# Kernel tuning notes

Measured on AMD Instinct MI355X. Metric: run time of the kernel, lower is better.

Reference implementation:

```python
import jax, jax.numpy as jnp
from jax import lax
import numpy as np

B, C, HH, WW = 8, 64, 128, 128
N = HH * WW
EPS = 1e-5


def _roll_h(xn, sign):
    # per-channel cyclic roll along H: out[b,c,h,w] = xn[b,c,(h - sign*c) % H, w]
    _, Cx, Hx, _ = xn.shape
    c = jnp.arange(Cx)[:, None]
    idx = (jnp.arange(Hx)[None, :] - sign * jnp.arange(Cx)[:, None]) % Hx  # (C,H)
    return xn[:, c, idx, :]


def _roll_w(xn, sign):
    return _roll_h(xn.transpose(0, 1, 3, 2), sign).transpose(0, 1, 3, 2)


def _ch_linear(xn, w, b):
    # nn.Linear over the channel dim of a BCHW tensor (token-MLP on (B,N,C))
    return jnp.einsum('bchw,cd->bdhw', xn, w) + b[None, :, None, None]


def _bn(xn, g, b):
    # BatchNorm2d, training-mode stats (biased var over B,H,W)
    m = xn.mean(axis=(0, 2, 3), keepdims=True)
    v = xn.var(axis=(0, 2, 3), keepdims=True)
    return (xn - m) * lax.rsqrt(v + EPS) * g[None, :, None, None] + b[None, :, None, None]


def _dwconv(xn, w, dil, pad):
    return lax.conv_general_dilated(xn, w, (1, 1), ((pad, pad), (pad, pad)),
                                    rhs_dilation=(dil, dil),
                                    dimension_numbers=('NCHW', 'OIHW', 'NCHW'),
                                    feature_group_count=xn.shape[1])


def _pc(xn, w):
    # 1x1 pointwise conv, no bias; w: (C_out, C_in)
    return jnp.einsum('bchw,oc->bohw', xn, w)


def lgff_forward(x, fc1_w, fc1_b, fc2_w, fc2_b, fc3_w, fc3_b, fc4_w, fc4_b,
                 fc5_w, fc5_b, ln_g, ln_b, pc_w, dw_w, dw_b, dw_bn_g, dw_bn_b,
                 dd_w, dd_bn_g, dd_bn_b, se_w1, se_b1, se_w2, se_b2, H, W):
    Bx, Nx, Cx = x.shape
    xn = x.transpose(0, 2, 1).reshape(Bx, Cx, H, W)
    # branch 1: roll+c along H -> fc1 -> GELU -> roll+c along W -> fc2
    a = jax.nn.gelu(_ch_linear(_roll_h(xn, 1), fc1_w, fc1_b), approximate=False)
    x_1 = _ch_linear(_roll_w(a, 1), fc2_w, fc2_b) + xn
    # branch 2: roll-c along W -> fc3 -> GELU -> roll+c along H -> fc4
    b = jax.nn.gelu(_ch_linear(_roll_w(xn, -1), fc3_w, fc3_b), approximate=False)
    x_2 = _ch_linear(_roll_h(b, 1), fc4_w, fc4_b) + xn
    # concat along feature dim (token layout dim=2 == channel dim here), LayerNorm(2C), fc5
    xc = jnp.concatenate([x_1, x_2], axis=1)  # (B, 2C, H, W)
    m = xc.mean(axis=1, keepdims=True)
    v = xc.var(axis=1, keepdims=True)
    xc = (xc - m) * lax.rsqrt(v + EPS) * ln_g[None, :, None, None] + ln_b[None, :, None, None]
    x1 = _ch_linear(xc, fc5_w, fc5_b) + xn
    # conv fusion part
    x2 = _pc(x1, pc_w)
    y = jax.nn.relu(_bn(_dwconv(x2, dw_w, 1, 1) + dw_b[None, :, None, None], dw_bn_g, dw_bn_b))
    y = jax.nn.relu(_bn(_dwconv(y, dd_w, 2, 2), dd_bn_g, dd_bn_b))
    y = _pc(y, pc_w)
    # four branches x3..x6 share identical weights/input -> identical outputs
    x7 = 4.0 * (x2 * y)
    # SE block
    s = x7.mean(axis=(2, 3), keepdims=True)  # (B,C,1,1)
    e = jax.nn.relu(jnp.einsum('bcij,oc->boij', s, se_w1) + se_b1[None, :, None, None])
    e = jax.nn.sigmoid(jnp.einsum('bcij,oc->boij', e, se_w2) + se_b2[None, :, None, None])
    return x7 + x7 * e  # (B, C, H, W)


def setup_inputs():
    key = jax.random.key(0)
    ks = jax.random.split(key, 12)
    r = C // 8
    inp = {
        'x': jax.random.normal(ks[0], (B, N, C), jnp.float32),
        'fc1_w': jax.random.normal(ks[1], (C, C), jnp.float32) * 0.02,
        'fc1_b': jnp.zeros((C,), jnp.float32),
        'fc2_w': jax.random.normal(ks[2], (C, C), jnp.float32) * 0.02,
        'fc2_b': jnp.zeros((C,), jnp.float32),
        'fc3_w': jax.random.normal(ks[3], (C, C), jnp.float32) * 0.02,
        'fc3_b': jnp.zeros((C,), jnp.float32),
        'fc4_w': jax.random.normal(ks[4], (C, C), jnp.float32) * 0.02,
        'fc4_b': jnp.zeros((C,), jnp.float32),
        'fc5_w': jax.random.normal(ks[5], (2 * C, C), jnp.float32) * 0.02,
        'fc5_b': jnp.zeros((C,), jnp.float32),
        'ln_g': jnp.ones((2 * C,), jnp.float32),
        'ln_b': jnp.zeros((2 * C,), jnp.float32),
        'pc_w': jax.random.normal(ks[6], (C, C), jnp.float32) * np.sqrt(2.0 / C).astype(np.float32),
        'dw_w': jax.random.normal(ks[7], (C, 1, 3, 3), jnp.float32) * np.sqrt(2.0 / 9.0).astype(np.float32),
        'dw_b': jnp.zeros((C,), jnp.float32),
        'dw_bn_g': jnp.ones((C,), jnp.float32),
        'dw_bn_b': jnp.zeros((C,), jnp.float32),
        'dd_w': jax.random.normal(ks[8], (C, 1, 3, 3), jnp.float32) * np.sqrt(2.0 / 9.0).astype(np.float32),
        'dd_bn_g': jnp.ones((C,), jnp.float32),
        'dd_bn_b': jnp.zeros((C,), jnp.float32),
        'se_w1': jax.random.normal(ks[9], (r, C), jnp.float32) * np.sqrt(2.0 / r).astype(np.float32),
        'se_b1': jnp.zeros((r,), jnp.float32),
        'se_w2': jax.random.normal(ks[10], (C, r), jnp.float32) * np.sqrt(2.0 / C).astype(np.float32),
        'se_b2': jnp.zeros((C,), jnp.float32),
        'H': HH,
        'W': WW,
    }
    return inp


def reference(x, fc1_w, fc1_b, fc2_w, fc2_b, fc3_w, fc3_b, fc4_w, fc4_b,
              fc5_w, fc5_b, ln_g, ln_b, pc_w, dw_w, dw_b, dw_bn_g, dw_bn_b,
              dd_w, dd_bn_g, dd_bn_b, se_w1, se_b1, se_w2, se_b2, H, W):
    return lgff_forward(x, fc1_w, fc1_b, fc2_w, fc2_b, fc3_w, fc3_b, fc4_w, fc4_b,
                        fc5_w, fc5_b, ln_g, ln_b, pc_w, dw_w, dw_b, dw_bn_g, dw_bn_b,
                        dd_w, dd_bn_g, dd_bn_b, se_w1, se_b1, se_w2, se_b2, H, W)
```

## Files before the change

kernel.cpp:

```cpp
#include <hip/hip_runtime.h>

constexpr int NB  = 8;
constexpr int NC  = 64;
constexpr int NH  = 128;
constexpr int NW  = 128;
constexpr int NHW = NH * NW;
constexpr int CHW = NC * NHW;
constexpr int SZ  = NB * CHW;
constexpr int NPOS = NB * NHW;
constexpr float EPS = 1e-5f;

typedef unsigned short u16;
using bf8   = __attribute__((ext_vector_type(8))) short;
using u16x8 = __attribute__((ext_vector_type(8))) u16;
using u16x4 = __attribute__((ext_vector_type(4))) u16;
using f32x4 = __attribute__((ext_vector_type(4))) float;

static __device__ inline short f2bf(float f) {
    union { float f; unsigned int u; } v; v.f = f;
    unsigned int r = v.u + 0x7fffu + ((v.u >> 16) & 1u);
    return (short)(r >> 16);
}
static __device__ inline float bf2f(u16 u) {
    union { unsigned int i; float f; } v; v.i = ((unsigned int)u) << 16;
    return v.f;
}

__global__ void k_transpose(const float* __restrict__ x, u16* __restrict__ xn,
                            const float* __restrict__ w5, const float* __restrict__ lng,
                            const float* __restrict__ lnb, float* __restrict__ PQ) {
    if (blockIdx.x == 2048) {
        int d = threadIdx.x;
        if (d < 64) {
            float P = 0.f, Q = 0.f;
            for (int c = 0; c < 128; ++c) {
                float wv = w5[c * 64 + d];
                P += lng[c] * wv;
                Q += lnb[c] * wv;
            }
            PQ[d] = P; PQ[64 + d] = Q;
        }
        return;
    }
    __shared__ float t[64 * 65];
    int b   = blockIdx.x >> 8;
    int hw0 = (blockIdx.x & 255) << 6;
    int tid = threadIdx.x;
    #pragma unroll
    for (int k = 0; k < 16; ++k) {
        int idx = tid + (k << 8);
        int c = idx & 63, hwl = idx >> 6;
        t[c * 65 + hwl] = x[((size_t)b * NHW + hw0 + hwl) * NC + c];
    }
    __syncthreads();
    #pragma unroll
    for (int k = 0; k < 16; ++k) {
        int idx = tid + (k << 8);
        int hwl = idx & 63, c = idx >> 6;
        xn[(size_t)(b * NC + c) * NHW + hw0 + hwl] = (u16)f2bf(t[c * 65 + hwl]);
    }
}

__global__ __launch_bounds__(512) void
k_mfc2(const u16* __restrict__ xn,
       const float* __restrict__ w1, const float* __restrict__ b1,
       const float* __restrict__ w3, const float* __restrict__ b3,
       u16* __restrict__ t1, u16* __restrict__ t2) {
    __shared__ short wA[64 * 64];
    __shared__ short wB[64 * 64];
    int tid = threadIdx.x;
    int l = tid & 63, wv = tid >> 6;
    int q = l >> 4, col = l & 15;
    int bid = ((blockIdx.x & 7) << 7) | (blockIdx.x >> 3);

    {
        const float* wsrc = (wv < 4) ? w1 : w3;
        short* wdst = (wv < 4) ? wA : wB;
        int wv4 = wv & 3;
        #pragma unroll
        for (int i = 0; i < 8; ++i) {
            int c0 = wv4 * 2 + i * 8;
            unsigned int pk = (unsigned int)(u16)f2bf(wsrc[c0 * 64 + l]) |
                              ((unsigned int)(u16)f2bf(wsrc[(c0 + 1) * 64 + l]) << 16);
            *(unsigned int*)&wdst[l * 64 + (c0 ^ ((l & 7) << 3))] = pk;
        }
    }
    __syncthreads();

    int p  = bid * 128 + wv * 16 + col;
    int b  = p >> 14;
    int hw = p & (NHW - 1);
    int h  = hw >> 7, w = hw & 127;
    const u16* inb = xn + (size_t)b * CHW;

    f32x4 acc1[4], acc2[4];
    #pragma unroll
    for (int dt = 0; dt < 4; ++dt) {
        acc1[dt] = (f32x4){0.f, 0.f, 0.f, 0.f};
        acc2[dt] = (f32x4){0.f, 0.f, 0.f, 0.f};
    }
    #pragma unroll
    for (int ks = 0; ks < 2; ++ks) {
        bf8 f1, f2;
        #pragma unroll
        for (int j = 0; j < 8; ++j) {
            int c = ks * 32 + q * 8 + j;
            f1[j] = (short)inb[c * NHW + (((h - c) & 127) << 7) + w];
            f2[j] = (short)inb[c * NHW + (h << 7) + ((w + c) & 127)];
        }
        #pragma unroll
        for (int dt = 0; dt < 4; ++dt) {
            int d = dt * 16 + col;
            int wo = (ks * 32 + q * 8) ^ ((d & 7) << 3);
            acc1[dt] = __builtin_amdgcn_mfma_f32_16x16x32_bf16(f1, *(bf8*)&wA[d * 64 + wo], acc1[dt], 0, 0, 0);
            acc2[dt] = __builtin_amdgcn_mfma_f32_16x16x32_bf16(f2, *(bf8*)&wB[d * 64 + wo], acc2[dt], 0, 0, 0);
        }
    }

    int hwst = (bid * 128 + wv * 16 + q * 4) & (NHW - 1);
    size_t ob = (size_t)b * CHW + hwst;
    #pragma unroll
    for (int dt = 0; dt < 4; ++dt) {
        int d = dt * 16 + col;
        float bb1 = b1[d], bb3 = b3[d];
        u16x4 o1v, o2v;
        #pragma unroll
        for (int r = 0; r < 4; ++r) {
            float v1 = acc1[dt][r] + bb1;
            v1 = 0.5f * v1 * (1.f + erff(v1 * 0.70710678118654752f));
            float v2 = acc2[dt][r] + bb3;
            v2 = 0.5f * v2 * (1.f + erff(v2 * 0.70710678118654752f));
            o1v[r] = (u16)f2bf(v1);
            o2v[r] = (u16)f2bf(v2);
        }
        *(u16x4*)&t1[ob + (size_t)d * NHW] = o1v;
        *(u16x4*)&t2[ob + (size_t)d * NHW] = o2v;
    }
}

__global__ __launch_bounds__(512) void
k_ffuse(const u16* __restrict__ t1, const u16* __restrict__ t2,
        const u16* __restrict__ xnb,
        const float* __restrict__ fc2w, const float* __restrict__ fc2b,
        const float* __restrict__ fc4w, const float* __restrict__ fc4b,
        const float* __restrict__ w5, const float* __restrict__ lng,
        const float* __restrict__ PQ, const float* __restrict__ b5,
        u16* __restrict__ x1out) {
    __shared__ short wA[64 * 64];
    __shared__ short wB[64 * 64];
    __shared__ short wG[64 * 128];
    __shared__ short xt[128 * 140];

    int tid = threadIdx.x;
    int l = tid & 63, wv = tid >> 6;
    int q = l >> 4, col = l & 15;
    int bid = ((blockIdx.x & 7) << 7) | (blockIdx.x >> 3);

    {
        const float* wsrc = (wv < 4) ? fc2w : fc4w;
        short* wdst = (wv < 4) ? wA : wB;
        int wv4 = wv & 3;
        #pragma unroll
        for (int i = 0; i < 8; ++i) {
            int c0 = wv4 * 2 + i * 8;
            unsigned int pk = (unsigned int)(u16)f2bf(wsrc[c0 * 64 + l]) |
                              ((unsigned int)(u16)f2bf(wsrc[(c0 + 1) * 64 + l]) << 16);
            *(unsigned int*)&wdst[l * 64 + (c0 ^ ((l & 7) << 3))] = pk;
        }
    }
    #pragma unroll
    for (int i = 0; i < 8; ++i) {
        int c0 = wv * 2 + i * 16;
        unsigned int pk = (unsigned int)(u16)f2bf(lng[c0] * w5[c0 * 64 + l]) |
                          ((unsigned int)(u16)f2bf(lng[c0 + 1] * w5[(c0 + 1) * 64 + l]) << 16);
        *(unsigned int*)&wG[l * 128 + (c0 ^ ((l & 7) << 3))] = pk;
    }
    __syncthreads();

    int p  = bid * 128 + wv * 16 + col;
    int b  = p >> 14;
    int hw = p & (NHW - 1);
    int h  = hw >> 7, w = hw & 127;
    size_t base = (size_t)b * CHW;

    f32x4 acc1[4], acc2[4];
    #pragma unroll
    for (int dt = 0; dt < 4; ++dt) {
        acc1[dt] = (f32x4){0.f, 0.f, 0.f, 0.f};
        acc2[dt] = (f32x4){0.f, 0.f, 0.f, 0.f};
    }
    #pragma unroll
    for (int ks = 0; ks < 2; ++ks) {
        bf8 f1, f2;
        #pragma unroll
        for (int j = 0; j < 8; ++j) {
            int c = ks * 32 + q * 8 + j;
            f1[j] = (short)t1[base + c * NHW + (h << 7) + ((w - c) & 127)];
            f2[j] = (short)t2[base + c * NHW + (((h - c) & 127) << 7) + w];
        }
        #pragma unroll
        for (int dt = 0; dt < 4; ++dt) {
            int d = dt * 16 + col;
            int wo = (ks * 32 + q * 8) ^ ((d & 7) << 3);
            acc1[dt] = __builtin_amdgcn_mfma_f32_16x16x32_bf16(f1, *(bf8*)&wA[d * 64 + wo], acc1[dt], 0, 0, 0);
            acc2[dt] = __builtin_amdgcn_mfma_f32_16x16x32_bf16(f2, *(bf8*)&wB[d * 64 + wo], acc2[dt], 0, 0, 0);
        }
    }

    int hwst = (bid * 128 + wv * 16 + q * 4) & (NHW - 1);
    size_t ob = base + hwst;
    u16x4 xr4[4];
    #pragma unroll
    for (int dt = 0; dt < 4; ++dt)
        xr4[dt] = *(const u16x4*)&xnb[ob + (size_t)(dt * 16 + col) * NHW];

    float s[4] = {0.f, 0.f, 0.f, 0.f}, sq[4] = {0.f, 0.f, 0.f, 0.f};
    int posr = wv * 16 + q * 4;
    #pragma unroll
    for (int dt = 0; dt < 4; ++dt) {
        int d = dt * 16 + col;
        float bb2 = fc2b[d], bb4 = fc4b[d];
        #pragma unroll
        for (int r = 0; r < 4; ++r) {
            float xv = bf2f(xr4[dt][r]);
            float v1 = acc1[dt][r] + bb2 + xv;
            float v2 = acc2[dt][r] + bb4 + xv;
            s[r]  += v1 + v2;
            sq[r] += v1 * v1 + v2 * v2;
            xt[(posr + r) * 140 + d]      = f2bf(v1);
            xt[(posr + r) * 140 + 64 + d] = f2bf(v2);
        }
    }
    #pragma unroll
    for (int off = 1; off < 16; off <<= 1) {
        #pragma unroll
        for (int r = 0; r < 4; ++r) {
            s[r]  += __shfl_xor(s[r], off);
            sq[r] += __shfl_xor(sq[r], off);
        }
    }
    float rstd[4], mr[4];
    #pragma unroll
    for (int r = 0; r < 4; ++r) {
        float m   = s[r] * (1.f / 128.f);
        float var = sq[r] * (1.f / 128.f) - m * m;
        rstd[r] = rsqrtf(var + EPS);
        mr[r]   = m * rstd[r];
    }
    __syncthreads();

    f32x4 acc[4];
    #pragma unroll
    for (int dt = 0; dt < 4; ++dt) acc[dt] = (f32x4){0.f, 0.f, 0.f, 0.f};
    #pragma unroll
    for (int ks = 0; ks < 4; ++ks) {
        bf8 bfr = *(bf8*)&xt[(wv * 16 + col) * 140 + ks * 32 + q * 8];
        #pragma unroll
        for (int dt = 0; dt < 4; ++dt) {
            int d = dt * 16 + col;
            bf8 wfr = *(bf8*)&wG[d * 128 + ((ks * 32 + q * 8) ^ ((d & 7) << 3))];
            acc[dt] = __builtin_amdgcn_mfma_f32_16x16x32_bf16(bfr, wfr, acc[dt], 0, 0, 0);
        }
    }

    #pragma unroll
    for (int dt = 0; dt < 4; ++dt) {
        int d = dt * 16 + col;
        float pqd = PQ[d], pqq = PQ[64 + d], b5d = b5[d];
        u16x4 ov;
        #pragma unroll
        for (int r = 0; r < 4; ++r) {
            float val = rstd[r] * acc[dt][r] + pqq - mr[r] * pqd + b5d + bf2f(xr4[dt][r]);
            ov[r] = (u16)f2bf(val);
        }
        *(u16x4*)&x1out[ob + (size_t)d * NHW] = ov;
    }
}

template<bool BNRELU_IN, bool SEPART>
__global__ __launch_bounds__(512) void
k_mfc(const u16* __restrict__ in, const float* __restrict__ wgt,
      const float* __restrict__ psum, const float* __restrict__ psq,
      const float* __restrict__ bng, const float* __restrict__ bnb,
      const u16* __restrict__ x2in, float* __restrict__ gpart,
      u16* __restrict__ out) {
    __shared__ short wt[64 * 64];
    __shared__ float scl[64], sft[64];
    __shared__ float spart[8][64];
    int tid = threadIdx.x;
    int l = tid & 63, wv = tid >> 6;
    int q = l >> 4, col = l & 15;
    int bid = ((blockIdx.x & 7) << 7) | (blockIdx.x >> 3);

    #pragma unroll
    for (int i = 0; i < 8; ++i) {
        int d = wv * 8 + i;
        wt[d * 64 + (l ^ ((d & 7) << 3))] = f2bf(wgt[d * 64 + l]);
    }
    if (BNRELU_IN && tid < 64) {
        float s = 0.f, qv = 0.f;
        #pragma unroll
        for (int i = 0; i < 32; ++i) {
            int bb = i >> 2, j = i & 3;
            int idx = ((bb * 64 + tid) << 2) + j;
            s += psum[idx]; qv += psq[idx];
        }
        const float inv = 1.f / (float)(NB * NHW);
        float m = s * inv;
        float var = qv * inv - m * m;
        float rs = rsqrtf(var + EPS);
        float sc = rs * bng[tid];
        scl[tid] = sc;
        sft[tid] = bnb[tid] - m * sc;
    }
    __syncthreads();

    int p  = bid * 128 + wv * 16 + col;
    int b  = p >> 14;
    int hw = p & (NHW - 1);
    const u16* inb = in + (size_t)b * CHW;

    f32x4 acc[4];
    #pragma unroll
    for (int dt = 0; dt < 4; ++dt) acc[dt] = (f32x4){0.f, 0.f, 0.f, 0.f};

    #pragma unroll
    for (int ks = 0; ks < 2; ++ks) {
        bf8 bfr;
        #pragma unroll
        for (int j = 0; j < 8; ++j) {
            int c = ks * 32 + q * 8 + j;
            u16 raw = inb[c * NHW + hw];
            if (BNRELU_IN) {
                float v = fmaxf(bf2f(raw) * scl[c] + sft[c], 0.f);
                bfr[j] = f2bf(v);
            } else {
                bfr[j] = (short)raw;
            }
        }
        #pragma unroll
        for (int dt = 0; dt < 4; ++dt) {
            int d = dt * 16 + col;
            bf8 afr = *(bf8*)&wt[d * 64 + ((ks * 32 + q * 8) ^ ((d & 7) << 3))];
            acc[dt] = __builtin_amdgcn_mfma_f32_16x16x32_bf16(bfr, afr, acc[dt], 0, 0, 0);
        }
    }

    int hwst = (bid * 128 + wv * 16 + q * 4) & (NHW - 1);
    size_t ob = (size_t)b * CHW + hwst;
    float pp[4] = {0.f, 0.f, 0.f, 0.f};
    #pragma unroll
    for (int dt = 0; dt < 4; ++dt) {
        int d = dt * 16 + col;
        u16x4 ov;
        #pragma unroll
        for (int r = 0; r < 4; ++r) ov[r] = (u16)f2bf(acc[dt][r]);
        *(u16x4*)&out[ob + (size_t)d * NHW] = ov;
        if (SEPART) {
            u16x4 xv = *(const u16x4*)&x2in[ob + (size_t)d * NHW];
            #pragma unroll
            for (int r = 0; r < 4; ++r) pp[dt] += bf2f(xv[r]) * bf2f(ov[r]);
        }
    }

    if (SEPART) {
        #pragma unroll
        for (int dt = 0; dt < 4; ++dt) {
            pp[dt] += __shfl_xor(pp[dt], 16);
            pp[dt] += __shfl_xor(pp[dt], 32);
        }
        if (l < 16) {
            #pragma unroll
            for (int dt = 0; dt < 4; ++dt) spart[wv][dt * 16 + l] = pp[dt];
        }
        __syncthreads();
        if (tid < 64) {
            float s = 0.f;
            #pragma unroll
            for (int w8 = 0; w8 < 8; ++w8) s += spart[w8][tid];
            gpart[(size_t)bid * 64 + tid] = s;
        }
    }
}

__global__ void k_se_fin(const float* __restrict__ gpart, float* __restrict__ svec) {
    int b = blockIdx.x, c = threadIdx.x;
    float s = 0.f;
    for (int k = 0; k < 128; ++k) s += gpart[(size_t)(b * 128 + k) * 64 + c];
    svec[b * 64 + c] = s * (4.f / (float)NHW);
}

template<int DIL, bool HASBIAS, bool BNIN>
__global__ __launch_bounds__(256) void
k_dwlds(const u16* __restrict__ in, const float* __restrict__ wgt,
        const float* __restrict__ bias,
        const float* __restrict__ psumIn, const float* __restrict__ psqIn,
        const float* __restrict__ bng, const float* __restrict__ bnb,
        u16* __restrict__ out, float* __restrict__ psumOut, float* __restrict__ psqOut) {
    constexpr int STR = 136;
    __shared__ float tile[36 * STR];
    __shared__ float ss[256], sq[256];

    int blk = ((blockIdx.x & 7) << 8) | (blockIdx.x >> 3);
    int q   = blk & 3;
    int bc  = blk >> 2;
    int c   = bc & 63;
    int r0  = q * 32;
    int tid = threadIdx.x;
    const u16* ip = in + (size_t)bc * NHW;

    float scale = 0.f, shift = 0.f;
    if (BNIN) {
        float s = 0.f, qv = 0.f;
        #pragma unroll
        for (int i = 0; i < 32; ++i) {
            int bb = i >> 2, j = i & 3;
            int idx = ((bb * 64 + c) << 2) + j;
            s += psumIn[idx]; qv += psqIn[idx];
        }
        const float inv = 1.f / (float)(NB * NHW);
        float m = s * inv;
        float var = qv * inv - m * m;
        float rs = rsqrtf(var + EPS);
        scale = rs * bng[c];
        shift = bnb[c] - m * scale;
    }

    #pragma unroll 1
    for (int idx = tid; idx < 36 * 16; idx += 256) {
        int lr = idx >> 4, u = idx & 15;
        int gr = r0 - 2 + lr;
        float v[8] = {0.f, 0.f, 0.f, 0.f, 0.f, 0.f, 0.f, 0.f};
        if (gr >= 0 && gr < NH) {
            u16x8 raw = *(const u16x8*)(ip + gr * NW + u * 8);
            #pragma unroll
            for (int j = 0; j < 8; ++j) {
                float f = bf2f(raw[j]);
                if (BNIN) f = fmaxf(f * scale + shift, 0.f);
                v[j] = f;
            }
        }
        *(float4*)&tile[lr * STR + 4 + u * 8]     = make_float4(v[0], v[1], v[2], v[3]);
        *(float4*)&tile[lr * STR + 4 + u * 8 + 4] = make_float4(v[4], v[5], v[6], v[7]);
        if (u == 0)  *(float4*)&tile[lr * STR]       = make_float4(0.f, 0.f, 0.f, 0.f);
        if (u == 15) *(float4*)&tile[lr * STR + 132] = make_float4(0.f, 0.f, 0.f, 0.f);
    }
    __syncthreads();

    float wc[9];
    #pragma unroll
    for (int k = 0; k < 9; ++k) wc[k] = wgt[c * 9 + k];

    int row  = tid >> 3;
    int col0 = (tid & 7) * 16;
    float o[16];
    float bb = HASBIAS ? bias[c] : 0.f;
    #pragma unroll
    for (int j = 0; j < 16; ++j) o[j] = bb;

    #pragma unroll
    for (int i = 0; i < 3; ++i) {
        const float* rp = &tile[(row + 2 + (i - 1) * DIL) * STR + 4 + col0];
        float4 A  = *(const float4*)(rp - 4);
        float4 B0 = *(const float4*)(rp);
        float4 B1 = *(const float4*)(rp + 4);
        float4 B2 = *(const float4*)(rp + 8);
        float4 B3 = *(const float4*)(rp + 12);
        float4 Cc = *(const float4*)(rp + 16);
        float ww[24] = {A.x,A.y,A.z,A.w, B0.x,B0.y,B0.z,B0.w, B1.x,B1.y,B1.z,B1.w,
                        B2.x,B2.y,B2.z,B2.w, B3.x,B3.y,B3.z,B3.w, Cc.x,Cc.y,Cc.z,Cc.w};
        float w0 = wc[3 * i], w1 = wc[3 * i + 1], w2 = wc[3 * i + 2];
        #pragma unroll
        for (int j = 0; j < 16; ++j)
            o[j] += w0 * ww[4 + j - DIL] + w1 * ww[4 + j] + w2 * ww[4 + j + DIL];
    }

    u16* op = out + (size_t)bc * NHW + (r0 + row) * NW + col0;
    u16x8 o1, o2;
    #pragma unroll
    for (int j = 0; j < 8; ++j) { o1[j] = (u16)f2bf(o[j]); o2[j] = (u16)f2bf(o[8 + j]); }
    *(u16x8*)(op)     = o1;
    *(u16x8*)(op + 8) = o2;

    float s = 0.f, qq = 0.f;
    #pragma unroll
    for (int j = 0; j < 16; ++j) { s += o[j]; qq += o[j] * o[j]; }
    ss[tid] = s; sq[tid] = qq; __syncthreads();
    for (int off = 128; off > 0; off >>= 1) {
        if (tid < off) { ss[tid] += ss[tid + off]; sq[tid] += sq[tid + off]; }
        __syncthreads();
    }
    if (tid == 0) { psumOut[blk] = ss[0]; psqOut[blk] = sq[0]; }
}

__global__ void k_final8(const u16* __restrict__ x2, const u16* __restrict__ y3,
                         const float* __restrict__ svec,
                         const float* __restrict__ w1, const float* __restrict__ b1,
                         const float* __restrict__ w2, const float* __restrict__ b2,
                         float* __restrict__ out) {
    __shared__ float sh[64], e1[8], ev[1];
    int tid = threadIdx.x;
    int bc = blockIdx.x >> 3;
    int b  = bc >> 6, c = bc & 63;

    if (tid < 64) sh[tid] = svec[b * 64 + tid];
    __syncthreads();
    if (tid < 8) {
        float a = b1[tid];
        for (int cc = 0; cc < 64; ++cc) a += sh[cc] * w1[tid * 64 + cc];
        e1[tid] = a > 0.f ? a : 0.f;
    }
    __syncthreads();
    if (tid == 0) {
        float a = b2[c];
        #pragma unroll
        for (int j = 0; j < 8; ++j) a += e1[j] * w2[c * 8 + j];
        ev[0] = 1.f / (1.f + expf(-a));
    }
    __syncthreads();

    int t = blockIdx.x * 256 + tid;
    float f = 4.f * (1.f + ev[0]);
    u16x8 av = *(const u16x8*)(x2 + (size_t)t * 8);
    u16x8 bv = *(const u16x8*)(y3 + (size_t)t * 8);
    float4 o0, o1;
    o0.x = f * bf2f(av[0]) * bf2f(bv[0]); o0.y = f * bf2f(av[1]) * bf2f(bv[1]);
    o0.z = f * bf2f(av[2]) * bf2f(bv[2]); o0.w = f * bf2f(av[3]) * bf2f(bv[3]);
    o1.x = f * bf2f(av[4]) * bf2f(bv[4]); o1.y = f * bf2f(av[5]) * bf2f(bv[5]);
    o1.z = f * bf2f(av[6]) * bf2f(bv[6]); o1.w = f * bf2f(av[7]) * bf2f(bv[7]);
    *(float4*)(out + (size_t)t * 8)     = o0;
    *(float4*)(out + (size_t)t * 8 + 4) = o1;
}

extern "C" void kernel_launch(void* const* d_in, const int* in_sizes, int n_in,
                              void* d_out, int out_size, void* d_ws, size_t ws_size,
                              hipStream_t stream) {
    const float* x     = (const float*)d_in[0];
    const float* fc1w  = (const float*)d_in[1];
    const float* fc1b  = (const float*)d_in[2];
    const float* fc2w  = (const float*)d_in[3];
    const float* fc2b  = (const float*)d_in[4];
    const float* fc3w  = (const float*)d_in[5];
    const float* fc3b  = (const float*)d_in[6];
    const float* fc4w  = (const float*)d_in[7];
    const float* fc4b  = (const float*)d_in[8];
    const float* fc5w  = (const float*)d_in[9];
    const float* fc5b  = (const float*)d_in[10];
    const float* lng   = (const float*)d_in[11];
    const float* lnb   = (const float*)d_in[12];
    const float* pcw   = (const float*)d_in[13];
    const float* dww   = (const float*)d_in[14];
    const float* dwb   = (const float*)d_in[15];
    const float* dwbng = (const float*)d_in[16];
    const float* dwbnb = (const float*)d_in[17];
    const float* ddw   = (const float*)d_in[18];
    const float* ddbng = (const float*)d_in[19];
    const float* ddbnb = (const float*)d_in[20];
    const float* sew1  = (const float*)d_in[21];
    const float* seb1  = (const float*)d_in[22];
    const float* sew2  = (const float*)d_in[23];
    const float* seb2  = (const float*)d_in[24];

    float* out = (float*)d_out;
    u16* wsu = (u16*)d_ws;
    u16* bufA = wsu;
    u16* bufB = wsu + (size_t)SZ;
    u16* bufC = wsu + (size_t)2 * SZ;
    u16* bufD = wsu + (size_t)3 * SZ;
    float* st = (float*)(wsu + (size_t)4 * SZ);
    float* psumA = st;
    float* psqA  = st + 2048;
    float* psumB = st + 4096;
    float* psqB  = st + 6144;
    float* svec  = st + 8192;
    float* pqv   = st + 8704;
    float* gpart = st + 8832;

    dim3 blk(256);
    dim3 blk512(512);
    const float* nil = nullptr;
    const u16*   nilu = nullptr;
    float*       nilf = nullptr;

    k_transpose<<<2049, blk, 0, stream>>>(x, bufA, fc5w, lng, lnb, pqv);
    k_mfc2<<<NPOS / 128, blk512, 0, stream>>>(bufA, fc1w, fc1b, fc3w, fc3b, bufB, bufC);
    k_ffuse<<<NPOS / 128, blk512, 0, stream>>>(bufB, bufC, bufA, fc2w, fc2b, fc4w, fc4b,
                                               fc5w, lng, pqv, fc5b, bufD);
    k_mfc<false, false><<<NPOS / 128, blk512, 0, stream>>>(bufD, pcw, nil, nil, nil, nil, nilu, nilf, bufA);
    k_dwlds<1, true, false><<<2048, blk, 0, stream>>>(bufA, dww, dwb, nil, nil, nil, nil, bufB, psumA, psqA);
    k_dwlds<2, false, true><<<2048, blk, 0, stream>>>(bufB, ddw, nil, psumA, psqA, dwbng, dwbnb, bufC, psumB, psqB);
    k_mfc<true, true><<<NPOS / 128, blk512, 0, stream>>>(bufC, pcw, psumB, psqB, ddbng, ddbnb, bufA, gpart, bufD);
    k_se_fin<<<NB, 64, 0, stream>>>(gpart, svec);
    k_final8<<<SZ / 2048, blk, 0, stream>>>(bufA, bufD, svec, sew1, seb1, sew2, seb2, out);
}
```

Baseline: 138.9 us.

## Recompute first depthwise conv inside fused dilated-conv kernel; fold product into pc epilogue

The first depthwise conv now runs only to gather BatchNorm statistics and no longer writes its output. A new fused kernel recomputes that conv with a one-row halo, applies BN+ReLU in shared memory, then runs the dilated conv, so one full intermediate tensor is never written or read back. The final pointwise-conv epilogue also multiplies by x2 (times 4) before storing, so the last kernel reads one tensor instead of two. In exchange the first conv is computed twice and the fused kernel needs more shared memory, which may lower occupancy.

```diff
diff --git a/kernel.cpp b/kernel.cpp
--- a/kernel.cpp
+++ b/kernel.cpp
@@ -353,14 +353,20 @@
     for (int dt = 0; dt < 4; ++dt) {
         int d = dt * 16 + col;
         u16x4 ov;
-        #pragma unroll
-        for (int r = 0; r < 4; ++r) ov[r] = (u16)f2bf(acc[dt][r]);
-        *(u16x4*)&out[ob + (size_t)d * NHW] = ov;
         if (SEPART) {
             u16x4 xv = *(const u16x4*)&x2in[ob + (size_t)d * NHW];
             #pragma unroll
-            for (int r = 0; r < 4; ++r) pp[dt] += bf2f(xv[r]) * bf2f(ov[r]);
-        }
+            for (int r = 0; r < 4; ++r) {
+                float x2v = bf2f(xv[r]);
+                float y3v = acc[dt][r];
+                pp[dt] += x2v * y3v;
+                ov[r] = (u16)f2bf(4.f * x2v * y3v);
+            }
+        } else {
+            #pragma unroll
+            for (int r = 0; r < 4; ++r) ov[r] = (u16)f2bf(acc[dt][r]);
+        }
+        *(u16x4*)&out[ob + (size_t)d * NHW] = ov;
     }
 
     if (SEPART) {
@@ -390,13 +396,11 @@
     svec[b * 64 + c] = s * (4.f / (float)NHW);
 }
 
-template<int DIL, bool HASBIAS, bool BNIN>
+template<bool STORE>
 __global__ __launch_bounds__(256) void
-k_dwlds(const u16* __restrict__ in, const float* __restrict__ wgt,
-        const float* __restrict__ bias,
-        const float* __restrict__ psumIn, const float* __restrict__ psqIn,
-        const float* __restrict__ bng, const float* __restrict__ bnb,
-        u16* __restrict__ out, float* __restrict__ psumOut, float* __restrict__ psqOut) {
+k_dwlds1(const u16* __restrict__ in, const float* __restrict__ wgt,
+         const float* __restrict__ bias,
+         u16* __restrict__ out, float* __restrict__ psumOut, float* __restrict__ psqOut) {
     constexpr int STR = 136;
     __shared__ float tile[36 * STR];
     __shared__ float ss[256], sq[256];
@@ -408,23 +412,6 @@
     int r0  = q * 32;
     int tid = threadIdx.x;
     const u16* ip = in + (size_t)bc * NHW;
-
-    float scale = 0.f, shift = 0.f;
-    if (BNIN) {
-        float s = 0.f, qv = 0.f;
-        #pragma unroll
-        for (int i = 0; i < 32; ++i) {
-            int bb = i >> 2, j = i & 3;
-            int idx = ((bb * 64 + c) << 2) + j;
-            s += psumIn[idx]; qv += psqIn[idx];
-        }
-        const float inv = 1.f / (float)(NB * NHW);
-        float m = s * inv;
-        float var = qv * inv - m * m;
-        float rs = rsqrtf(var + EPS);
-        scale = rs * bng[c];
-        shift = bnb[c] - m * scale;
-    }
 
     #pragma unroll 1
     for (int idx = tid; idx < 36 * 16; idx += 256) {
@@ -434,11 +421,7 @@
         if (gr >= 0 && gr < NH) {
             u16x8 raw = *(const u16x8*)(ip + gr * NW + u * 8);
             #pragma unroll
-            for (int j = 0; j < 8; ++j) {
-                float f = bf2f(raw[j]);
-                if (BNIN) f = fmaxf(f * scale + shift, 0.f);
-                v[j] = f;
-            }
+            for (int j = 0; j < 8; ++j) v[j] = bf2f(raw[j]);
         }
         *(float4*)&tile[lr * STR + 4 + u * 8]     = make_float4(v[0], v[1], v[2], v[3]);
         *(float4*)&tile[lr * STR + 4 + u * 8 + 4] = make_float4(v[4], v[5], v[6], v[7]);
@@ -454,13 +437,13 @@
     int row  = tid >> 3;
     int col0 = (tid & 7) * 16;
     float o[16];
-    float bb = HASBIAS ? bias[c] : 0.f;
+    float bb = bias[c];
     #pragma unroll
     for (int j = 0; j < 16; ++j) o[j] = bb;
 
     #pragma unroll
     for (int i = 0; i < 3; ++i) {
-        const float* rp = &tile[(row + 2 + (i - 1) * DIL) * STR + 4 + col0];
+        const float* rp = &tile[(row + 2 + (i - 1)) * STR + 4 + col0];
         float4 A  = *(const float4*)(rp - 4);
         float4 B0 = *(const float4*)(rp);
         float4 B1 = *(const float4*)(rp + 4);
@@ -472,15 +455,17 @@
         float w0 = wc[3 * i], w1 = wc[3 * i + 1], w2 = wc[3 * i + 2];
         #pragma unroll
         for (int j = 0; j < 16; ++j)
-            o[j] += w0 * ww[4 + j - DIL] + w1 * ww[4 + j] + w2 * ww[4 + j + DIL];
-    }
-
-    u16* op = out + (size_t)bc * NHW + (r0 + row) * NW + col0;
-    u16x8 o1, o2;
-    #pragma unroll
-    for (int j = 0; j < 8; ++j) { o1[j] = (u16)f2bf(o[j]); o2[j] = (u16)f2bf(o[8 + j]); }
-    *(u16x8*)(op)     = o1;
-    *(u16x8*)(op + 8) = o2;
+            o[j] += w0 * ww[4 + j - 1] + w1 * ww[4 + j] + w2 * ww[4 + j + 1];
+    }
+
+    if (STORE) {
+        u16* op = out + (size_t)bc * NHW + (r0 + row) * NW + col0;
+        u16x8 o1, o2;
+        #pragma unroll
+        for (int j = 0; j < 8; ++j) { o1[j] = (u16)f2bf(o[j]); o2[j] = (u16)f2bf(o[8 + j]); }
+        *(u16x8*)(op)     = o1;
+        *(u16x8*)(op + 8) = o2;
+    }
 
     float s = 0.f, qq = 0.f;
     #pragma unroll
@@ -493,7 +478,138 @@
     if (tid == 0) { psumOut[blk] = ss[0]; psqOut[blk] = sq[0]; }
 }
 
-__global__ void k_final8(const u16* __restrict__ x2, const u16* __restrict__ y3,
+__global__ __launch_bounds__(256) void
+k_dwfuse(const u16* __restrict__ x2, const float* __restrict__ dww,
+         const float* __restrict__ dwb,
+         const float* __restrict__ psumIn, const float* __restrict__ psqIn,
+         const float* __restrict__ bng, const float* __restrict__ bnb,
+         const float* __restrict__ ddw,
+         u16* __restrict__ out, float* __restrict__ psumOut, float* __restrict__ psqOut) {
+    constexpr int STR = 136;
+    __shared__ float tile1[38 * STR];
+    __shared__ float tile2[36 * STR];
+    __shared__ float ss[256], sq[256];
+
+    int blk = ((blockIdx.x & 7) << 8) | (blockIdx.x >> 3);
+    int q   = blk & 3;
+    int bc  = blk >> 2;
+    int c   = bc & 63;
+    int r0  = q * 32;
+    int tid = threadIdx.x;
+    const u16* ip = x2 + (size_t)bc * NHW;
+
+    float scale, shift;
+    {
+        float s = 0.f, qv = 0.f;
+        #pragma unroll
+        for (int i = 0; i < 32; ++i) {
+            int bb = i >> 2, j = i & 3;
+            int idx = ((bb * 64 + c) << 2) + j;
+            s += psumIn[idx]; qv += psqIn[idx];
+        }
+        const float inv = 1.f / (float)(NB * NHW);
+        float m = s * inv;
+        float var = qv * inv - m * m;
+        float rs = rsqrtf(var + EPS);
+        scale = rs * bng[c];
+        shift = bnb[c] - m * scale;
+    }
+
+    #pragma unroll 1
+    for (int idx = tid; idx < 38 * 16; idx += 256) {
+        int lr = idx >> 4, u = idx & 15;
+        int gr = r0 - 3 + lr;
+        float v[8] = {0.f, 0.f, 0.f, 0.f, 0.f, 0.f, 0.f, 0.f};
+        if (gr >= 0 && gr < NH) {
+            u16x8 raw = *(const u16x8*)(ip + gr * NW + u * 8);
+            #pragma unroll
+            for (int j = 0; j < 8; ++j) v[j] = bf2f(raw[j]);
+        }
+        *(float4*)&tile1[lr * STR + 4 + u * 8]     = make_float4(v[0], v[1], v[2], v[3]);
+        *(float4*)&tile1[lr * STR + 4 + u * 8 + 4] = make_float4(v[4], v[5], v[6], v[7]);
+        if (u == 0)  *(float4*)&tile1[lr * STR]       = make_float4(0.f, 0.f, 0.f, 0.f);
+        if (u == 15) *(float4*)&tile1[lr * STR + 132] = make_float4(0.f, 0.f, 0.f, 0.f);
+    }
+    __syncthreads();
+
+    float wc1[9], wc2[9];
+    #pragma unroll
+    for (int k = 0; k < 9; ++k) { wc1[k] = dww[c * 9 + k]; wc2[k] = ddw[c * 9 + k]; }
+    float dbias = dwb[c];
+
+    #pragma unroll 1
+    for (int idx = tid; idx < 36 * 32; idx += 256) {
+        int lr2 = idx >> 5, w4 = idx & 31;
+        int gr2 = r0 - 2 + lr2;
+        float o0 = 0.f, o1 = 0.f, o2 = 0.f, o3 = 0.f;
+        if (gr2 >= 0 && gr2 < NH) {
+            o0 = o1 = o2 = o3 = dbias;
+            #pragma unroll
+            for (int i = 0; i < 3; ++i) {
+                const float* rp = &tile1[(lr2 + i) * STR + 4 + w4 * 4];
+                float4 A = *(const float4*)(rp - 4);
+                float4 M = *(const float4*)(rp);
+                float4 R = *(const float4*)(rp + 4);
+                float win[12] = {A.x,A.y,A.z,A.w, M.x,M.y,M.z,M.w, R.x,R.y,R.z,R.w};
+                float w0 = wc1[3 * i], w1 = wc1[3 * i + 1], w2 = wc1[3 * i + 2];
+                o0 += w0 * win[3] + w1 * win[4] + w2 * win[5];
+                o1 += w0 * win[4] + w1 * win[5] + w2 * win[6];
+                o2 += w0 * win[5] + w1 * win[6] + w2 * win[7];
+                o3 += w0 * win[6] + w1 * win[7] + w2 * win[8];
+            }
+            o0 = fmaxf(o0 * scale + shift, 0.f);
+            o1 = fmaxf(o1 * scale + shift, 0.f);
+            o2 = fmaxf(o2 * scale + shift, 0.f);
+            o3 = fmaxf(o3 * scale + shift, 0.f);
+        }
+        *(float4*)&tile2[lr2 * STR + 4 + w4 * 4] = make_float4(o0, o1, o2, o3);
+        if (w4 == 0)  *(float4*)&tile2[lr2 * STR]       = make_float4(0.f, 0.f, 0.f, 0.f);
+        if (w4 == 31) *(float4*)&tile2[lr2 * STR + 132] = make_float4(0.f, 0.f, 0.f, 0.f);
+    }
+    __syncthreads();
+
+    int row  = tid >> 3;
+    int col0 = (tid & 7) * 16;
+    float o[16];
+    #pragma unroll
+    for (int j = 0; j < 16; ++j) o[j] = 0.f;
+
+    #pragma unroll
+    for (int i = 0; i < 3; ++i) {
+        const float* rp = &tile2[(row + 2 + (i - 1) * 2) * STR + 4 + col0];
+        float4 A  = *(const float4*)(rp - 4);
+        float4 B0 = *(const float4*)(rp);
+        float4 B1 = *(const float4*)(rp + 4);
+        float4 B2 = *(const float4*)(rp + 8);
+        float4 B3 = *(const float4*)(rp + 12);
+        float4 Cc = *(const float4*)(rp + 16);
+        float ww[24] = {A.x,A.y,A.z,A.w, B0.x,B0.y,B0.z,B0.w, B1.x,B1.y,B1.z,B1.w,
+                        B2.x,B2.y,B2.z,B2.w, B3.x,B3.y,B3.z,B3.w, Cc.x,Cc.y,Cc.z,Cc.w};
+        float w0 = wc2[3 * i], w1 = wc2[3 * i + 1], w2 = wc2[3 * i + 2];
+        #pragma unroll
+        for (int j = 0; j < 16; ++j)
+            o[j] += w0 * ww[4 + j - 2] + w1 * ww[4 + j] + w2 * ww[4 + j + 2];
+    }
+
+    u16* op = out + (size_t)bc * NHW + (r0 + row) * NW + col0;
+    u16x8 o1v, o2v;
+    #pragma unroll
+    for (int j = 0; j < 8; ++j) { o1v[j] = (u16)f2bf(o[j]); o2v[j] = (u16)f2bf(o[8 + j]); }
+    *(u16x8*)(op)     = o1v;
+    *(u16x8*)(op + 8) = o2v;
+
+    float s = 0.f, qq = 0.f;
+    #pragma unroll
+    for (int j = 0; j < 16; ++j) { s += o[j]; qq += o[j] * o[j]; }
+    ss[tid] = s; sq[tid] = qq; __syncthreads();
+    for (int off = 128; off > 0; off >>= 1) {
+        if (tid < off) { ss[tid] += ss[tid + off]; sq[tid] += sq[tid + off]; }
+        __syncthreads();
+    }
+    if (tid == 0) { psumOut[blk] = ss[0]; psqOut[blk] = sq[0]; }
+}
+
+__global__ void k_final8(const u16* __restrict__ x7,
                          const float* __restrict__ svec,
                          const float* __restrict__ w1, const float* __restrict__ b1,
                          const float* __restrict__ w2, const float* __restrict__ b2,
@@ -520,14 +636,13 @@
     __syncthreads();
 
     int t = blockIdx.x * 256 + tid;
-    float f = 4.f * (1.f + ev[0]);
-    u16x8 av = *(const u16x8*)(x2 + (size_t)t * 8);
-    u16x8 bv = *(const u16x8*)(y3 + (size_t)t * 8);
+    float f = 1.f + ev[0];
+    u16x8 av = *(const u16x8*)(x7 + (size_t)t * 8);
     float4 o0, o1;
-    o0.x = f * bf2f(av[0]) * bf2f(bv[0]); o0.y = f * bf2f(av[1]) * bf2f(bv[1]);
-    o0.z = f * bf2f(av[2]) * bf2f(bv[2]); o0.w = f * bf2f(av[3]) * bf2f(bv[3]);
-    o1.x = f * bf2f(av[4]) * bf2f(bv[4]); o1.y = f * bf2f(av[5]) * bf2f(bv[5]);
-    o1.z = f * bf2f(av[6]) * bf2f(bv[6]); o1.w = f * bf2f(av[7]) * bf2f(bv[7]);
+    o0.x = f * bf2f(av[0]); o0.y = f * bf2f(av[1]);
+    o0.z = f * bf2f(av[2]); o0.w = f * bf2f(av[3]);
+    o1.x = f * bf2f(av[4]); o1.y = f * bf2f(av[5]);
+    o1.z = f * bf2f(av[6]); o1.w = f * bf2f(av[7]);
     *(float4*)(out + (size_t)t * 8)     = o0;
     *(float4*)(out + (size_t)t * 8 + 4) = o1;
 }
@@ -581,15 +696,17 @@
     const float* nil = nullptr;
     const u16*   nilu = nullptr;
     float*       nilf = nullptr;
+    u16*         nilw = nullptr;
 
     k_transpose<<<2049, blk, 0, stream>>>(x, bufA, fc5w, lng, lnb, pqv);
     k_mfc2<<<NPOS / 128, blk512, 0, stream>>>(bufA, fc1w, fc1b, fc3w, fc3b, bufB, bufC);
     k_ffuse<<<NPOS / 128, blk512, 0, stream>>>(bufB, bufC, bufA, fc2w, fc2b, fc4w, fc4b,
                                                fc5w, lng, pqv, fc5b, bufD);
     k_mfc<false, false><<<NPOS / 128, blk512, 0, stream>>>(bufD, pcw, nil, nil, nil, nil, nilu, nilf, bufA);
-    k_dwlds<1, true, false><<<2048, blk, 0, stream>>>(bufA, dww, dwb, nil, nil, nil, nil, bufB, psumA, psqA);
-    k_dwlds<2, false, true><<<2048, blk, 0, stream>>>(bufB, ddw, nil, psumA, psqA, dwbng, dwbnb, bufC, psumB, psqB);
+    k_dwlds1<false><<<2048, blk, 0, stream>>>(bufA, dww, dwb, nilw, psumA, psqA);
+    k_dwfuse<<<2048, blk, 0, stream>>>(bufA, dww, dwb, psumA, psqA, dwbng, dwbnb,
+                                       ddw, bufC, psumB, psqB);
     k_mfc<true, true><<<NPOS / 128, blk512, 0, stream>>>(bufC, pcw, psumB, psqB, ddbng, ddbnb, bufA, gpart, bufD);
     k_se_fin<<<NB, 64, 0, stream>>>(gpart, svec);
-    k_final8<<<SZ / 2048, blk, 0, stream>>>(bufA, bufD, svec, sew1, seb1, sew2, seb2, out);
-}
+    k_final8<<<SZ / 2048, blk, 0, stream>>>(bufD, svec, sew1, seb1, sew2, seb2, out);
+}
```

Result: no change. 138.0 us (-0.6%).
